# Performance work log

Hardware: AMD Instinct MI355X
Metric: run time of the kernel (lower is better)

Reference implementation:

```python
import jax, jax.numpy as jnp
import numpy as np

J = 24
PARENTS = np.array([-1, 0, 1, 2, 3, 0, 5, 6, 7, 0, 9, 10, 11, 12, 11, 14, 15, 16, 17, 11, 19, 20, 21, 22])
# ancestor-or-self matrix: A[i, j] = 1 if j is on the chain from root to joint i
_A = np.zeros((J, J), dtype=np.float32)
for _i in range(J):
    _j = _i
    while _j != -1:
        _A[_i, _j] = 1.0
        _j = PARENTS[_j]
ANCESTOR = jnp.asarray(_A)
PAR_CLAMPED = jnp.asarray(np.where(PARENTS < 0, 0, PARENTS))
ROOT_MASK = jnp.asarray((PARENTS >= 0).astype(np.float32))  # zero delta at root
SMPL_OFFSETS = np.array([[0.0, 0.0, 0.0], [-0.0112, 0.0372, -0.0522], [0.0051, 0.0276, -0.2453], [-0.0238, -0.0094, -0.271], [0.0775, 0.0261, -0.0383], [-0.0086, -0.0383, -0.0575], [-0.0031, -0.0275, -0.2436], [-0.0219, 0.0121, -0.2666], [0.0827, -0.0221, -0.0394], [-0.0244, 0.0028, 0.079], [0.017, 0.0028, 0.0876], [0.0018, -0.0014, 0.0356], [-0.0212, -0.0085, 0.1343], [0.032, 0.0064, 0.0565], [-0.012, 0.0455, 0.0724], [-0.0121, 0.078, 0.0287], [-0.0146, 0.1621, -0.0099], [-0.0047, 0.1687, 0.0081], [-0.0099, 0.055, -0.0068], [-0.015, -0.0527, 0.0714], [-0.0054, -0.0719, 0.0297], [-0.0198, -0.1651, -0.0091], [-0.0038, -0.1708, 0.0043], [-0.0064, -0.0563, -0.0055]], dtype=np.float32)
G = jnp.asarray(np.array([[0, 1, 0], [0, 0, 1], [1, 0, 0]], dtype=np.float32))


def setup_inputs() -> dict:
    key = jax.random.key(0)
    B = 131072
    orientations = jax.random.normal(key, (B, J, 3, 3), dtype=jnp.float32)
    offsets = jnp.asarray(SMPL_OFFSETS)
    return {"orientations": orientations, "offsets": offsets}


def reference(orientations, offsets):
    # to_mvnx frame change: G^T @ R @ G, per joint
    o = jnp.einsum('kj,bnkl,lm->bnjm', G, orientations, G)  # [B,J,3,3]
    # per-joint bone delta in global frame: R_parent @ offset_child
    Rp = o[:, PAR_CLAMPED]                                   # [B,J,3,3]
    delta = jnp.einsum('bjkl,jl->bjk', Rp, offsets)          # [B,J,3]
    delta = delta * ROOT_MASK[None, :, None]
    # accumulate along static tree: position_i = sum of deltas of ancestors-or-self
    pos = jnp.einsum('ij,bjk->bik', ANCESTOR, delta)          # [B,J,3]
    # to_smpl: rotate positions back, equivalent to pos @ G^T
    return jnp.einsum('bjk,mk->bjm', pos, G)
```

## Files before the change

### kernel.cpp

```cpp
#include <hip/hip_runtime.h>

#define NJ  24
#define BPB 64
#define TPB 256
#define RST 217
#define OST 73

__global__ __launch_bounds__(TPB) void smpl_fk_kernel(
    const float* __restrict__ orient,
    const float* __restrict__ offs,
    float* __restrict__ out)
{
    constexpr int PAR[NJ] = {-1, 0, 1, 2, 3, 0, 5, 6, 7, 0, 9, 10, 11,
                             12, 11, 14, 15, 16, 17, 11, 19, 20, 21, 22};

    __shared__ float lds[BPB * RST];
    __shared__ float soff[NJ * 3];

    const int tid = threadIdx.x;
    const long long b0 = (long long)blockIdx.x * BPB;

    if (tid < NJ * 3) soff[tid] = offs[tid];

    const float4* gin = (const float4*)(orient + b0 * (NJ * 9));
    #pragma unroll
    for (int i = 0; i < 14; ++i) {
        int f4 = i * TPB + tid;
        if (f4 < BPB * 54) {
            float4 v = gin[f4];
            int b = f4 / 54;
            int w = f4 % 54;
            float* dst = &lds[b * RST + w * 4];
            dst[0] = v.x; dst[1] = v.y; dst[2] = v.z; dst[3] = v.w;
        }
    }
    __syncthreads();

    float pos[NJ][3];
    if (tid < BPB) {
        const float* Rb = &lds[tid * RST];
        pos[0][0] = 0.f; pos[0][1] = 0.f; pos[0][2] = 0.f;
        #pragma unroll
        for (int j = 1; j < NJ; ++j) {
            const int p = PAR[j];
            const float o0 = soff[j * 3 + 1];
            const float o1 = soff[j * 3 + 2];
            const float o2 = soff[j * 3 + 0];
            #pragma unroll
            for (int m = 0; m < 3; ++m) {
                const float r0 = Rb[p * 9 + m * 3 + 0];
                const float r1 = Rb[p * 9 + m * 3 + 1];
                const float r2 = Rb[p * 9 + m * 3 + 2];
                pos[j][m] = fmaf(r0, o0, fmaf(r1, o1, fmaf(r2, o2, pos[p][m])));
            }
        }
    }
    __syncthreads();

    if (tid < BPB) {
        float* ob = &lds[tid * OST];
        #pragma unroll
        for (int j = 0; j < NJ; ++j) {
            ob[j * 3 + 0] = pos[j][0];
            ob[j * 3 + 1] = pos[j][1];
            ob[j * 3 + 2] = pos[j][2];
        }
    }
    __syncthreads();

    float* gout = out + b0 * (NJ * 3);
    #pragma unroll
    for (int i = 0; i < 18; ++i) {
        int idx = i * TPB + tid;
        int b = idx / 72;
        int w = idx % 72;
        gout[idx] = lds[b * OST + w];
    }
}

extern "C" void kernel_launch(void* const* d_in, const int* in_sizes, int n_in,
                              void* d_out, int out_size, void* d_ws, size_t ws_size,
                              hipStream_t stream) {
    const float* orient = (const float*)d_in[0];
    const float* offs   = (const float*)d_in[1];
    float* out          = (float*)d_out;

    const int B = in_sizes[0] / (NJ * 9);
    const int blocks = (B + BPB - 1) / BPB;
    smpl_fk_kernel<<<blocks, TPB, 0, stream>>>(orient, offs, out);
}
```

Before: 181.5 us.

## Split FK compute across three threads per batch row and halve block batch

```diff
diff --git a/kernel.cpp b/kernel.cpp
--- a/kernel.cpp
+++ b/kernel.cpp
@@ -1,7 +1,7 @@
 #include <hip/hip_runtime.h>
 
 #define NJ  24
-#define BPB 64
+#define BPB 32
 #define TPB 256
 #define RST 217
 #define OST 73
@@ -24,7 +24,7 @@
 
     const float4* gin = (const float4*)(orient + b0 * (NJ * 9));
     #pragma unroll
-    for (int i = 0; i < 14; ++i) {
+    for (int i = 0; i < 7; ++i) {
         int f4 = i * TPB + tid;
         if (f4 < BPB * 54) {
             float4 v = gin[f4];
@@ -36,41 +36,34 @@
     }
     __syncthreads();
 
-    float pos[NJ][3];
-    if (tid < BPB) {
-        const float* Rb = &lds[tid * RST];
-        pos[0][0] = 0.f; pos[0][1] = 0.f; pos[0][2] = 0.f;
+    float pos[NJ];
+    if (tid < BPB * 3) {
+        const int b = tid & (BPB - 1);
+        const int m = tid >> 5;
+        const float* Rb = &lds[b * RST + m * 3];
+        pos[0] = 0.f;
         #pragma unroll
         for (int j = 1; j < NJ; ++j) {
             const int p = PAR[j];
-            const float o0 = soff[j * 3 + 1];
-            const float o1 = soff[j * 3 + 2];
-            const float o2 = soff[j * 3 + 0];
-            #pragma unroll
-            for (int m = 0; m < 3; ++m) {
-                const float r0 = Rb[p * 9 + m * 3 + 0];
-                const float r1 = Rb[p * 9 + m * 3 + 1];
-                const float r2 = Rb[p * 9 + m * 3 + 2];
-                pos[j][m] = fmaf(r0, o0, fmaf(r1, o1, fmaf(r2, o2, pos[p][m])));
-            }
+            pos[j] = fmaf(Rb[p * 9 + 0], soff[j * 3 + 1],
+                     fmaf(Rb[p * 9 + 1], soff[j * 3 + 2],
+                     fmaf(Rb[p * 9 + 2], soff[j * 3 + 0], pos[p])));
         }
     }
     __syncthreads();
 
-    if (tid < BPB) {
-        float* ob = &lds[tid * OST];
+    if (tid < BPB * 3) {
+        const int b = tid & (BPB - 1);
+        const int m = tid >> 5;
+        float* ob = &lds[b * OST + m];
         #pragma unroll
-        for (int j = 0; j < NJ; ++j) {
-            ob[j * 3 + 0] = pos[j][0];
-            ob[j * 3 + 1] = pos[j][1];
-            ob[j * 3 + 2] = pos[j][2];
-        }
+        for (int j = 0; j < NJ; ++j) ob[j * 3] = pos[j];
     }
     __syncthreads();
 
     float* gout = out + b0 * (NJ * 3);
     #pragma unroll
-    for (int i = 0; i < 18; ++i) {
+    for (int i = 0; i < 9; ++i) {
         int idx = i * TPB + tid;
         int b = idx / 72;
         int w = idx % 72;
```

After: 179.7 us. No clear change (-1.0%).
